# Kernel optimization log

Measured on AMD Instinct MI355X. Metric: run time of the kernel, lower is better.

The kernel has to match this reference:

```python
import jax, jax.numpy as jnp
import numpy as np

N_NODES = 40000
N_EDGES = 640000
N_GRAPHS = 64
D = 128


def setup_inputs() -> dict:
    key = jax.random.key(0)
    ks = jax.random.split(key, 8)
    x = jax.random.normal(ks[0], (N_NODES, D), dtype=jnp.float32)
    edge_index = jax.random.randint(ks[1], (2, N_EDGES), 0, N_NODES, dtype=jnp.int64)
    batch = jnp.sort(jax.random.randint(ks[2], (N_NODES,), 0, N_GRAPHS, dtype=jnp.int64))
    s = 1.0 / np.sqrt(D)
    W_rel1 = jax.random.normal(ks[3], (D, D), dtype=jnp.float32) * s
    W_root1 = jax.random.normal(ks[4], (D, D), dtype=jnp.float32) * s
    W_rel2 = jax.random.normal(ks[5], (D, D), dtype=jnp.float32) * s
    W_root2 = jax.random.normal(ks[6], (D, D), dtype=jnp.float32) * s
    Wc = jax.random.normal(ks[7], (D, D), dtype=jnp.float32) * s
    b1 = jnp.zeros((D,), jnp.float32)
    b2 = jnp.zeros((D,), jnp.float32)
    bc = jnp.zeros((D,), jnp.float32)
    return dict(x=x, edge_index=edge_index, batch=batch,
                W_rel1=W_rel1, W_root1=W_root1, b1=b1,
                W_rel2=W_rel2, W_root2=W_root2, b2=b2,
                Wc=Wc, bc=bc)


def _graph_conv(x, src, dst, W_rel, W_root, b):
    # PyG GraphConv with mean aggregation:
    # out_i = W_rel @ mean_{j in N(i)} x_j + W_root @ x_i + b
    n = x.shape[0]
    msg = x[src]                                              # [E, D] gather
    agg = jax.ops.segment_sum(msg, dst, num_segments=n)       # [N, D]
    deg = jax.ops.segment_sum(jnp.ones_like(dst, dtype=x.dtype), dst, num_segments=n)
    agg = agg / jnp.maximum(deg, 1.0)[:, None]                # mean, 0 if isolated
    return agg @ W_rel.T + x @ W_root.T + b


def reference(x, edge_index, batch, W_rel1, W_root1, b1, W_rel2, W_root2, b2, Wc, bc):
    src, dst = edge_index[0], edge_index[1]
    h = jax.nn.relu(_graph_conv(x, src, dst, W_rel1, W_root1, b1))
    h = jax.nn.relu(_graph_conv(h, src, dst, W_rel2, W_root2, b2))
    # global_mean_pool (dropout is identity in eval mode)
    sums = jax.ops.segment_sum(h, batch, num_segments=N_GRAPHS)          # [G, D]
    cnts = jax.ops.segment_sum(jnp.ones_like(batch, dtype=h.dtype), batch, num_segments=N_GRAPHS)
    pooled = sums / jnp.maximum(cnts, 1.0)[:, None]
    return pooled @ Wc.T + bc
```

## Files before the change

kernel.cpp:

```cpp
#include <hip/hip_runtime.h>

#define DD 128
#define ANODE 4
#define SLOT 64

typedef __attribute__((ext_vector_type(8))) short short8v;
typedef __attribute__((ext_vector_type(4))) float float4v;

static __device__ __forceinline__ unsigned short f2bf(float f) {
  unsigned int u = __float_as_uint(f);
  u = (u + 0x7fffu + ((u >> 16) & 1u)) >> 16;
  return (unsigned short)u;
}
static __device__ __forceinline__ float blo(unsigned int u) {
  return __uint_as_float(u << 16);
}
static __device__ __forceinline__ float bhi(unsigned int u) {
  return __uint_as_float(u & 0xffff0000u);
}
static __device__ __forceinline__ unsigned int pk(float lo, float hi) {
  return (unsigned int)f2bf(lo) | ((unsigned int)f2bf(hi) << 16);
}

__global__ void prep_kernel(int* __restrict__ cnt, float* __restrict__ sums,
                            int ncnt, int nsums) {
  int i = blockIdx.x * blockDim.x + threadIdx.x;
  if (i < ncnt) cnt[i] = 0;
  if (i < nsums) sums[i] = 0.f;
}

__global__ void build_kernel(const int* __restrict__ src, const int* __restrict__ dst,
                             int* __restrict__ cnt, unsigned short* __restrict__ slot,
                             int E, int eb, int xb,
                             const float* __restrict__ x, unsigned short* __restrict__ XH,
                             int N,
                             const float* __restrict__ Wr1, const float* __restrict__ Wo1,
                             const float* __restrict__ Wr2, const float* __restrict__ Wo2,
                             unsigned short* __restrict__ Bpk) {
  int b = blockIdx.x;
  if (b < eb) {
    int e = b * 256 + threadIdx.x;
    if (e < E) {
      int s = src[e];
      int d = dst[e];
      int p = atomicAdd(&cnt[d], 1);
      if (p < SLOT) slot[(size_t)d * SLOT + p] = (unsigned short)s;
    }
  } else if (b < eb + xb) {
    int i = (b - eb) * 256 + threadIdx.x;
    if (i < N * 32) {
      float4 v = reinterpret_cast<const float4*>(x)[i];
      ushort4 h;
      h.x = f2bf(v.x); h.y = f2bf(v.y); h.z = f2bf(v.z); h.w = f2bf(v.w);
      reinterpret_cast<ushort4*>(XH)[i] = h;
    }
  } else {
    int i = (b - eb - xb) * 256 + threadIdx.x;
    if (i < 8192) {
      int L = i >> 12, rest = i & 4095;
      int kt = rest >> 9, nt = (rest >> 6) & 7, lane = rest & 63;
      int d = nt * 16 + (lane & 15);
      int kbase = kt * 32 + (lane >> 4) * 8;
      const float* Wrel = L ? Wr2 : Wr1;
      const float* Wroot = L ? Wo2 : Wo1;
      unsigned short* o = Bpk + (size_t)i * 8;
      #pragma unroll
      for (int j = 0; j < 8; ++j) {
        int k = kbase + j;
        float w = (k < DD) ? Wrel[d * DD + k] : Wroot[d * DD + (k - DD)];
        o[j] = f2bf(w);
      }
    }
  }
}

__global__ __launch_bounds__(256) void gather3(
    const uint4* __restrict__ X4, const unsigned short* __restrict__ slot,
    const int* __restrict__ cnt, uint4* __restrict__ AH4, int N) {
  int node = blockIdx.x * ANODE + (threadIdx.x >> 6);
  if (node >= N) return;
  int lane = threadIdx.x & 63;
  int sub = lane >> 4;
  int sl = lane & 15;
  int dg = cnt[node];
  if (dg > SLOT) dg = SLOT;
  const unsigned short* csr = slot + (size_t)node * SLOT;
  int pe = dg;
  float a0 = 0.f, a1 = 0.f, a2 = 0.f, a3 = 0.f, a4 = 0.f, a5 = 0.f, a6 = 0.f, a7 = 0.f;
  int p = 0;
  for (; p + 8 <= pe; p += 8) {
    int s0 = csr[p + sub];
    int s1 = csr[p + 4 + sub];
    uint4 u0 = X4[(size_t)s0 * 16 + sl];
    uint4 u1 = X4[(size_t)s1 * 16 + sl];
    a0 += blo(u0.x) + blo(u1.x);  a1 += bhi(u0.x) + bhi(u1.x);
    a2 += blo(u0.y) + blo(u1.y);  a3 += bhi(u0.y) + bhi(u1.y);
    a4 += blo(u0.z) + blo(u1.z);  a5 += bhi(u0.z) + bhi(u1.z);
    a6 += blo(u0.w) + blo(u1.w);  a7 += bhi(u0.w) + bhi(u1.w);
  }
  for (; p < pe; p += 4) {
    int q = p + sub;
    bool act = q < pe;
    int s0 = act ? (int)csr[q] : 0;
    uint4 u0 = X4[(size_t)s0 * 16 + sl];
    if (act) {
      a0 += blo(u0.x); a1 += bhi(u0.x);
      a2 += blo(u0.y); a3 += bhi(u0.y);
      a4 += blo(u0.z); a5 += bhi(u0.z);
      a6 += blo(u0.w); a7 += bhi(u0.w);
    }
  }
  #define RED2(v) v += __shfl_xor(v, 16, 64); v += __shfl_xor(v, 32, 64);
  RED2(a0) RED2(a1) RED2(a2) RED2(a3) RED2(a4) RED2(a5) RED2(a6) RED2(a7)
  #undef RED2
  float inv = 1.f / fmaxf((float)dg, 1.f);
  a0 *= inv; a1 *= inv; a2 *= inv; a3 *= inv;
  a4 *= inv; a5 *= inv; a6 *= inv; a7 *= inv;
  if (sub == 0) {
    uint4 h;
    h.x = pk(a0, a1); h.y = pk(a2, a3); h.z = pk(a4, a5); h.w = pk(a6, a7);
    AH4[(size_t)node * 16 + sl] = h;
  }
}

__global__ __launch_bounds__(128) void gemm2(
    const unsigned short* __restrict__ AH, const unsigned short* __restrict__ XH,
    const unsigned short* __restrict__ Bpk, const float* __restrict__ bias,
    unsigned short* __restrict__ HH,
    float* __restrict__ sums, const int* __restrict__ batch, int N) {
  int lane = threadIdx.x & 63;
  int wid = threadIdx.x >> 6;
  int m0 = (blockIdx.x * 2 + wid) * 16;
  if (m0 >= N) return;
  int arow = m0 + (lane & 15);
  if (arow >= N) arow = N - 1;
  int koff = (lane >> 4) * 8;
  const short8v* Bf = (const short8v*)Bpk;
  float4v acc[8];
  #pragma unroll
  for (int nt = 0; nt < 8; ++nt) acc[nt] = (float4v){0.f, 0.f, 0.f, 0.f};

  #pragma unroll
  for (int kt = 0; kt < 8; ++kt) {
    const unsigned short* hb = (kt < 4)
        ? (AH + (size_t)arow * DD + kt * 32 + koff)
        : (XH + (size_t)arow * DD + (kt - 4) * 32 + koff);
    short8v a = *reinterpret_cast<const short8v*>(hb);
    #pragma unroll
    for (int nt = 0; nt < 8; ++nt) {
      short8v b = Bf[(kt * 8 + nt) * 64 + lane];
      acc[nt] = __builtin_amdgcn_mfma_f32_16x16x32_bf16(a, b, acc[nt], 0, 0, 0);
    }
  }

  int col0 = lane & 15;
  int rbase = m0 + (lane >> 4) * 4;
  if (sums) {
    int gl = batch[m0];
    int me = (m0 + 15 < N) ? m0 + 15 : N - 1;
    int gh = batch[me];
    bool fast = (gl == gh) && (m0 + 16 <= N);
    #pragma unroll
    for (int nt = 0; nt < 8; ++nt) {
      int col = nt * 16 + col0;
      float bv = bias[col];
      float v0 = fmaxf(acc[nt][0] + bv, 0.f);
      float v1 = fmaxf(acc[nt][1] + bv, 0.f);
      float v2 = fmaxf(acc[nt][2] + bv, 0.f);
      float v3 = fmaxf(acc[nt][3] + bv, 0.f);
      if (fast) {
        float s = (v0 + v1) + (v2 + v3);
        s += __shfl_xor(s, 16, 64);
        s += __shfl_xor(s, 32, 64);
        if (lane < 16) atomicAdd(&sums[gl * DD + col], s);
      } else {
        float vv[4] = {v0, v1, v2, v3};
        #pragma unroll
        for (int r = 0; r < 4; ++r) {
          int row = rbase + r;
          if (row < N) atomicAdd(&sums[batch[row] * DD + col], vv[r]);
        }
      }
    }
  } else {
    #pragma unroll
    for (int nt = 0; nt < 8; ++nt) {
      int col = nt * 16 + col0;
      float bv = bias[col];
      #pragma unroll
      for (int r = 0; r < 4; ++r) {
        int row = rbase + r;
        if (row < N) {
          float v = fmaxf(acc[nt][r] + bv, 0.f);
          HH[(size_t)row * DD + col] = f2bf(v);
        }
      }
    }
  }
}

__global__ void final_kernel(const float* __restrict__ sums, const int* __restrict__ batch,
                             const float* __restrict__ Wc, const float* __restrict__ bc,
                             float* __restrict__ out, int N, int G) {
  int g = blockIdx.x;
  int d = threadIdx.x;
  __shared__ float p[DD];
  __shared__ float invs;
  if (d == 0) {
    int lo = 0, hi = N;
    while (lo < hi) { int m = (lo + hi) >> 1; if (batch[m] < g) lo = m + 1; else hi = m; }
    int a = lo;
    lo = 0; hi = N;
    while (lo < hi) { int m = (lo + hi) >> 1; if (batch[m] < g + 1) lo = m + 1; else hi = m; }
    invs = 1.0f / fmaxf((float)(lo - a), 1.0f);
  }
  __syncthreads();
  p[d] = sums[g * DD + d] * invs;
  __syncthreads();
  float acc = bc[d];
  #pragma unroll 8
  for (int k = 0; k < DD; ++k) acc += p[k] * Wc[d * DD + k];
  out[g * DD + d] = acc;
}

extern "C" void kernel_launch(void* const* d_in, const int* in_sizes, int n_in,
                              void* d_out, int out_size, void* d_ws, size_t ws_size,
                              hipStream_t stream) {
  const float* x   = (const float*)d_in[0];
  const int*   ei  = (const int*)d_in[1];
  const int* batch = (const int*)d_in[2];
  const float* Wr1 = (const float*)d_in[3];
  const float* Wo1 = (const float*)d_in[4];
  const float* b1  = (const float*)d_in[5];
  const float* Wr2 = (const float*)d_in[6];
  const float* Wo2 = (const float*)d_in[7];
  const float* b2  = (const float*)d_in[8];
  const float* Wc  = (const float*)d_in[9];
  const float* bc  = (const float*)d_in[10];
  float* out = (float*)d_out;

  const int N = in_sizes[0] / DD;
  const int E = in_sizes[1] / 2;
  const int G = out_size / DD;
  const int* src = ei;
  const int* dst = ei + E;

  const int Npad = (N + 63) & ~63;
  int* cnt = (int*)d_ws;
  unsigned short* slot = (unsigned short*)(cnt + Npad);
  float* sums = (float*)(slot + (size_t)N * SLOT);
  unsigned short* Bpk = (unsigned short*)(sums + (size_t)G * DD);

  unsigned short* XH = Bpk + 65536;
  unsigned short* HH = XH + (size_t)N * DD;
  unsigned short* AH = HH + (size_t)N * DD;

  const int blk = 256;
  int prep_threads = (Npad > G * DD) ? Npad : G * DD;
  prep_kernel<<<(prep_threads + blk - 1) / blk, blk, 0, stream>>>(cnt, sums, Npad, G * DD);

  int eb = (E + blk - 1) / blk;
  int xb = (N * 32 + blk - 1) / blk;
  build_kernel<<<eb + xb + 32, blk, 0, stream>>>(src, dst, cnt, slot, E, eb, xb,
                                                 x, XH, N, Wr1, Wo1, Wr2, Wo2, Bpk);

  int agg_blocks = (N + ANODE - 1) / ANODE;
  int gemm_blocks = (N + 31) / 32;

  gather3<<<agg_blocks, 256, 0, stream>>>((const uint4*)XH, slot, cnt, (uint4*)AH, N);
  gemm2<<<gemm_blocks, 128, 0, stream>>>(AH, XH, Bpk, b1, HH, nullptr, nullptr, N);
  gather3<<<agg_blocks, 256, 0, stream>>>((const uint4*)HH, slot, cnt, (uint4*)AH, N);
  gemm2<<<gemm_blocks, 128, 0, stream>>>(AH, HH, Bpk + 32768, b2, nullptr, sums, batch, N);

  final_kernel<<<G, DD, 0, stream>>>(sums, batch, Wc, bc, out, N, G);
}
```

Before: 139.3 us.

## Privatize edge-bucket counters into per-block-group copies, then merge

Edge insertion now spreads its atomics across 8 private copies of the per-node counters and slot arrays, chosen by block index. A new merge kernel then concatenates the copies into the final 64-slot adjacency. The aim is to reduce atomic contention and improve locality of the atomic traffic during graph build. In exchange it adds a kernel launch, a larger zeroing pass (8N counters), and extra memory traffic for the private slot buffers. Each copy is capped at 24 slots, so a heavily skewed node could lose edges. The path only runs when the workspace is large enough.

```diff
diff --git a/kernel.cpp b/kernel.cpp
--- a/kernel.cpp
+++ b/kernel.cpp
@@ -3,6 +3,8 @@
 #define DD 128
 #define ANODE 4
 #define SLOT 64
+#define CSLOT 24
+#define NC 8
 
 typedef __attribute__((ext_vector_type(8))) short short8v;
 typedef __attribute__((ext_vector_type(4))) float float4v;
@@ -22,15 +24,16 @@
   return (unsigned int)f2bf(lo) | ((unsigned int)f2bf(hi) << 16);
 }
 
-__global__ void prep_kernel(int* __restrict__ cnt, float* __restrict__ sums,
+__global__ void prep_kernel(int* __restrict__ cnta, float* __restrict__ sums,
                             int ncnt, int nsums) {
   int i = blockIdx.x * blockDim.x + threadIdx.x;
-  if (i < ncnt) cnt[i] = 0;
+  if (i < ncnt) cnta[i] = 0;
   if (i < nsums) sums[i] = 0.f;
 }
 
 __global__ void build_kernel(const int* __restrict__ src, const int* __restrict__ dst,
-                             int* __restrict__ cnt, unsigned short* __restrict__ slot,
+                             int* __restrict__ cnta, unsigned short* __restrict__ slota,
+                             int cslot, int priv,
                              int E, int eb, int xb,
                              const float* __restrict__ x, unsigned short* __restrict__ XH,
                              int N,
@@ -43,8 +46,9 @@
     if (e < E) {
       int s = src[e];
       int d = dst[e];
-      int p = atomicAdd(&cnt[d], 1);
-      if (p < SLOT) slot[(size_t)d * SLOT + p] = (unsigned short)s;
+      int idx = priv ? ((b & (NC - 1)) * N + d) : d;
+      int p = atomicAdd(&cnta[idx], 1);
+      if (p < cslot) slota[(size_t)idx * cslot + p] = (unsigned short)s;
     }
   } else if (b < eb + xb) {
     int i = (b - eb) * 256 + threadIdx.x;
@@ -72,6 +76,28 @@
       }
     }
   }
+}
+
+__global__ __launch_bounds__(256) void merge_kernel(
+    const int* __restrict__ cnt8, const unsigned short* __restrict__ slots8,
+    int* __restrict__ cnt, unsigned short* __restrict__ slot, int N) {
+  int wv = (blockIdx.x * 256 + threadIdx.x) >> 6;
+  int lane = threadIdx.x & 63;
+  if (wv >= N) return;
+  int total = 0;
+  #pragma unroll
+  for (int c = 0; c < NC; ++c) {
+    int k = cnt8[c * N + wv];
+    if (k > CSLOT) k = CSLOT;
+    if (lane < k) {
+      int pos = total + lane;
+      if (pos < SLOT)
+        slot[(size_t)wv * SLOT + pos] = slots8[(size_t)(c * N + wv) * CSLOT + lane];
+    }
+    total += k;
+  }
+  if (total > SLOT) total = SLOT;
+  if (lane == 0) cnt[wv] = total;
 }
 
 __global__ __launch_bounds__(256) void gather3(
@@ -255,14 +281,30 @@
   unsigned short* HH = XH + (size_t)N * DD;
   unsigned short* AH = HH + (size_t)N * DD;
 
+  unsigned short* tail = AH + (size_t)N * DD;
+  size_t priv_bytes = (size_t)NC * N * sizeof(int)
+                    + (size_t)NC * N * CSLOT * sizeof(unsigned short);
+  size_t used = (size_t)((char*)tail - (char*)d_ws);
+  int priv = (ws_size >= used + priv_bytes) ? 1 : 0;
+  int* cnt8 = priv ? (int*)tail : nullptr;
+  unsigned short* slots8 = priv ? (unsigned short*)(cnt8 + (size_t)NC * N) : nullptr;
+
   const int blk = 256;
-  int prep_threads = (Npad > G * DD) ? Npad : G * DD;
-  prep_kernel<<<(prep_threads + blk - 1) / blk, blk, 0, stream>>>(cnt, sums, Npad, G * DD);
+  int ncnt = priv ? NC * N : Npad;
+  int prep_threads = (ncnt > G * DD) ? ncnt : G * DD;
+  prep_kernel<<<(prep_threads + blk - 1) / blk, blk, 0, stream>>>(
+      priv ? cnt8 : cnt, sums, ncnt, G * DD);
 
   int eb = (E + blk - 1) / blk;
   int xb = (N * 32 + blk - 1) / blk;
-  build_kernel<<<eb + xb + 32, blk, 0, stream>>>(src, dst, cnt, slot, E, eb, xb,
-                                                 x, XH, N, Wr1, Wo1, Wr2, Wo2, Bpk);
+  if (priv) {
+    build_kernel<<<eb + xb + 32, blk, 0, stream>>>(
+        src, dst, cnt8, slots8, CSLOT, 1, E, eb, xb, x, XH, N, Wr1, Wo1, Wr2, Wo2, Bpk);
+    merge_kernel<<<(N * 64 + blk - 1) / blk, blk, 0, stream>>>(cnt8, slots8, cnt, slot, N);
+  } else {
+    build_kernel<<<eb + xb + 32, blk, 0, stream>>>(
+        src, dst, cnt, slot, SLOT, 0, E, eb, xb, x, XH, N, Wr1, Wo1, Wr2, Wo2, Bpk);
+  }
 
   int agg_blocks = (N + ANODE - 1) / ANODE;
   int gemm_blocks = (N + 31) / 32;
```

Result: slower. 164.4 us (+18.1%).
